# Optimization experiments

Measured on AMD Instinct MI355X. Metric: run time of the kernel, lower is better.

## Reference

```python
import jax, jax.numpy as jnp
import numpy as np

LEAKY_SLOPE = 0.2
MASK_VAL = -9e15


def setup_inputs() -> dict:
    key = jax.random.key(0)
    k1, k2, k3, k4, k5, k6 = jax.random.split(key, 6)
    N_ex, N_kc, F_in, F_out = 20000, 1024, 128, 128
    exercise_h = jax.random.normal(k1, (N_ex, F_in), dtype=jnp.float32)
    kc_h = jax.random.normal(k2, (N_kc, F_in), dtype=jnp.float32)
    adj_exercise_kc = jax.random.randint(k3, (N_ex, N_kc), 0, 2, dtype=jnp.int32)
    # learned params (kaiming-ish scale)
    W1 = jax.random.normal(k4, (F_in, F_out), dtype=jnp.float32) * np.sqrt(2.0 / F_in)
    E = jax.random.normal(k5, (F_in, F_out), dtype=jnp.float32) * np.sqrt(2.0 / F_in)
    a = jax.random.normal(k6, (2 * F_out, 1), dtype=jnp.float32) * np.sqrt(2.0 / (2 * F_out))
    return {"exercise_h": exercise_h, "kc_h": kc_h,
            "adj_exercise_kc": adj_exercise_kc, "W1": W1, "E": E, "a": a}


def reference(exercise_h, kc_h, adj_exercise_kc, W1, E, a):
    F_out = W1.shape[1]
    kc_Wh = kc_h @ W1              # [N_kc, F_out]
    ex_Wh = exercise_h @ W1        # [N_ex, F_out]
    # Decompose a into halves: cat([ex_Wh_i, kc_Wh_j]) @ a == ex_Wh_i@a1 + kc_Wh_j@a2.
    a1, a2 = a[:F_out, 0], a[F_out:, 0]
    e = jax.nn.leaky_relu(ex_Wh @ a1[:, None] + (kc_Wh @ a2)[None, :],
                          negative_slope=LEAKY_SLOPE)   # [N_ex, N_kc]
    e = jnp.where(adj_exercise_kc > 0, e, MASK_VAL)
    attention = jax.nn.softmax(e, axis=1)
    new_kc_embed = attention @ kc_Wh               # [N_ex, F_out]
    exercise_Eh = exercise_h @ E                   # mode == 2
    return jax.nn.elu(new_kc_embed * exercise_Eh)
```

## Files before the change

### kernel.cpp

```cpp
#include <hip/hip_runtime.h>
#include <math.h>

#define N_EXC   20000
#define N_KCC   1024
#define FDIM    128
#define LEAKY_S 0.2f

#define BR  32
#define TJ  64
#define EXS 136
#define WST 72

typedef unsigned short ushort_t;
typedef __attribute__((ext_vector_type(8))) short short8;
typedef __attribute__((ext_vector_type(4))) float floatx4;

__device__ __forceinline__ ushort_t f2bf(float f) {
    unsigned u = __float_as_uint(f);
    u += 0x7FFF + ((u >> 16) & 1);
    return (ushort_t)(u >> 16);
}

__device__ __forceinline__ void async16(const void* g, void* l) {
    __builtin_amdgcn_global_load_lds(
        (const __attribute__((address_space(1))) unsigned int*)g,
        (__attribute__((address_space(3))) unsigned int*)l,
        16, 0, 0);
}


__global__ __launch_bounds__(256) void gat_prep0(const float* __restrict__ W1,
                                                 const float* __restrict__ E,
                                                 const float* __restrict__ a,
                                                 float* __restrict__ ws)
{
    float* w1a1 = ws + N_KCC;
    ushort_t* kc_sw  = (ushort_t*)(ws + N_KCC + FDIM);
    ushort_t* E_sw   = kc_sw + FDIM * N_KCC;
    ushort_t* W1T_sw = E_sw + FDIM * FDIM;
    const int tid = threadIdx.x;

    if (blockIdx.x == 1) {
        #pragma unroll
        for (int u = 0; u < 8; ++u) {
            int ch = u * 256 + tid;
            int half = ch >> 10;
            int rem = ch & 1023;
            int n = rem >> 3, cpp = rem & 7;
            int c = cpp ^ (n & 7);
            int kbase = half * 64 + c * 8;
            unsigned pk[4];
            #pragma unroll
            for (int i = 0; i < 4; ++i) {
                float e0 = E[(kbase + 2 * i + 0) * FDIM + n];
                float e1 = E[(kbase + 2 * i + 1) * FDIM + n];
                pk[i] = (unsigned)f2bf(e0) | ((unsigned)f2bf(e1) << 16);
            }
            *(uint4*)(E_sw + ch * 8) = make_uint4(pk[0], pk[1], pk[2], pk[3]);
        }
        return;
    }

    __shared__ __align__(16) float w1f[128 * 132];
    __shared__ float a_lds[2 * FDIM];
    #pragma unroll
    for (int u = 0; u < 16; ++u) {
        int flat = u * 256 + tid;
        int k = flat >> 5, c4 = (flat & 31) * 4;
        float4 v = *(const float4*)(W1 + k * FDIM + c4);
        w1f[k * 132 + c4 + 0] = v.x; w1f[k * 132 + c4 + 1] = v.y;
        w1f[k * 132 + c4 + 2] = v.z; w1f[k * 132 + c4 + 3] = v.w;
    }
    a_lds[tid] = a[tid];
    __syncthreads();
    #pragma unroll
    for (int u = 0; u < 8; ++u) {
        int ch = u * 256 + tid;
        int f = ch >> 4, c = ch & 15;
        unsigned pk[4];
        #pragma unroll
        for (int i = 0; i < 4; ++i) {
            float v0 = w1f[(c * 8 + 2 * i + 0) * 132 + f];
            float v1 = w1f[(c * 8 + 2 * i + 1) * 132 + f];
            pk[i] = (unsigned)f2bf(v0) | ((unsigned)f2bf(v1) << 16);
        }
        *(uint4*)(W1T_sw + f * 128 + (c ^ (f & 15)) * 8) = make_uint4(pk[0], pk[1], pk[2], pk[3]);
    }
    if (tid < FDIM) {
        float acc = 0.f;
        #pragma unroll 8
        for (int f = 0; f < FDIM; ++f) acc += w1f[tid * 132 + f] * a_lds[f];
        w1a1[tid] = acc;
    }
}

__global__ __launch_bounds__(256) void gat_prep1(const float* __restrict__ kc_h,
                                                 const float* __restrict__ a,
                                                 float* __restrict__ ws)
{
    float* tarr = ws;
    ushort_t* kc_sw  = (ushort_t*)(ws + N_KCC + FDIM);
    ushort_t* E_sw   = kc_sw + FDIM * N_KCC;
    const ushort_t* W1T_sw = E_sw + FDIM * FDIM;

    __shared__ __align__(16) ushort_t w1t[128 * 128];
    __shared__ __align__(16) ushort_t outt[128 * 16];
    __shared__ float a2_lds[FDIM];
    __shared__ float scrT[256];

    const int tid = threadIdx.x;
    const int b = blockIdx.x;
    const int j0 = b * 16;
    const int jt = b >> 2;
    const int c0 = (b & 3) * 2;
    const int lane = tid & 63, w = tid >> 6;
    const int l15 = lane & 15, quad = lane >> 4;

    #pragma unroll
    for (int u = 0; u < 8; ++u) {
        int ci = u * 256 + tid;
        async16(W1T_sw + ci * 8, w1t + ci * 8);
    }
    if (tid < FDIM) a2_lds[tid] = a[FDIM + tid];

    short8 bfrag[4];
    #pragma unroll
    for (int kk = 0; kk < 4; ++kk) {
        const float* p = kc_h + (size_t)(j0 + l15) * FDIM + kk * 32 + quad * 8;
        float4 x = *(const float4*)(p);
        float4 y = *(const float4*)(p + 4);
        float v[8] = {x.x, x.y, x.z, x.w, y.x, y.y, y.z, y.w};
        unsigned pk[4];
        #pragma unroll
        for (int i = 0; i < 4; ++i)
            pk[i] = (unsigned)f2bf(v[2 * i]) | ((unsigned)f2bf(v[2 * i + 1]) << 16);
        uint4 q = make_uint4(pk[0], pk[1], pk[2], pk[3]);
        bfrag[kk] = *(const short8*)&q;
    }
    __syncthreads();

    floatx4 acc[2];
    acc[0] = (floatx4){0.f, 0.f, 0.f, 0.f};
    acc[1] = (floatx4){0.f, 0.f, 0.f, 0.f};
    #pragma unroll
    for (int kk = 0; kk < 4; ++kk) {
        #pragma unroll
        for (int g = 0; g < 2; ++g) {
            int f = w * 32 + g * 16 + l15;
            int cp = (kk * 4 + quad) ^ l15;
            short8 af = *(const short8*)(w1t + f * 128 + cp * 8);
            acc[g] = __builtin_amdgcn_mfma_f32_16x16x32_bf16(af, bfrag[kk], acc[g], 0, 0, 0);
        }
    }

    float tp = 0.f;
    #pragma unroll
    for (int g = 0; g < 2; ++g)
        #pragma unroll
        for (int reg = 0; reg < 4; ++reg) {
            int f = w * 32 + g * 16 + quad * 4 + reg;
            outt[f * 16 + l15] = f2bf(acc[g][reg]);
            tp += acc[g][reg] * a2_lds[f];
        }
    scrT[l15 * 16 + w * 4 + quad] = tp;
    __syncthreads();

    {
        int f = tid >> 1, hf = tid & 1;
        uint4 v = *(const uint4*)(outt + f * 16 + hf * 8);
        int cp = (c0 + hf) ^ (f & 7);
        *(uint4*)(kc_sw + (size_t)jt * 8192 + f * 64 + cp * 8) = v;
    }
    if (tid < 16) {
        float s = 0.f;
        #pragma unroll
        for (int p = 0; p < 16; ++p) s += scrT[tid * 16 + p];
        tarr[j0 + tid] = s;
    }
}

__global__ __launch_bounds__(256, 3) void gat_main(const float* __restrict__ ex_h,
                                                   const int* __restrict__ adj,
                                                   const float* __restrict__ ws,
                                                   float* __restrict__ out)
{
    const float* tarr = ws;
    const float* w1a1 = ws + N_KCC;
    const ushort_t* kc_sw = (const ushort_t*)(ws + N_KCC + FDIM);
    const ushort_t* E_sw  = kc_sw + FDIM * N_KCC;

    __shared__ __align__(16) float t_lds[N_KCC];
    __shared__ __align__(16) ushort_t kc_lds[2 * 8192];
    __shared__ __align__(16) ushort_t ww_lds[4608];
    __shared__ __align__(16) float scrA[256];
    __shared__ __align__(16) float scrB[256];
    __shared__ float w1a1_lds[FDIM];
    __shared__ float s_lds[BR], m_lds[BR], denom_lds[BR];

    const int tid  = threadIdx.x;
    const int R0   = blockIdx.x * BR;
    const int lane = tid & 63, wid = tid >> 6;
    const int l15  = lane & 15, quad = lane >> 4;

    #pragma unroll
    for (int u = 0; u < 8; ++u) {
        int ci = u * 256 + tid;
        async16(E_sw + ci * 8, kc_lds + ci * 8);
    }

    #pragma unroll
    for (int u = 0; u < 4; ++u) t_lds[u * 256 + tid] = tarr[u * 256 + tid];
    if (tid < FDIM) w1a1_lds[tid] = w1a1[tid];
    const int r0 = tid >> 3;
    const int fc = (tid & 7) * 16;
    float exv[16];
    {
        const float* src = ex_h + (size_t)(R0 + r0) * FDIM + fc;
        #pragma unroll
        for (int c = 0; c < 4; ++c) {
            float4 v = *(const float4*)(src + c * 4);
            exv[c * 4 + 0] = v.x; exv[c * 4 + 1] = v.y;
            exv[c * 4 + 2] = v.z; exv[c * 4 + 3] = v.w;
        }
        unsigned pk[8];
        #pragma unroll
        for (int i = 0; i < 8; ++i)
            pk[i] = (unsigned)f2bf(exv[2 * i]) | ((unsigned)f2bf(exv[2 * i + 1]) << 16);
        *(uint4*)(ww_lds + r0 * EXS + fc)     = make_uint4(pk[0], pk[1], pk[2], pk[3]);
        *(uint4*)(ww_lds + r0 * EXS + fc + 8) = make_uint4(pk[4], pk[5], pk[6], pk[7]);
    }

    const int r_w = tid >> 3;
    const int jg  = tid & 7;
    const int* abase = adj + (size_t)(R0 + r_w) * N_KCC + jg * 8;
    unsigned msk[4];
    #pragma unroll
    for (int g = 0; g < 4; ++g) {
        int4 q0 = *(const int4*)(abase + (g * 4 + 0) * 64);
        int4 q1 = *(const int4*)(abase + (g * 4 + 0) * 64 + 4);
        int4 q2 = *(const int4*)(abase + (g * 4 + 1) * 64);
        int4 q3 = *(const int4*)(abase + (g * 4 + 1) * 64 + 4);
        int4 q4 = *(const int4*)(abase + (g * 4 + 2) * 64);
        int4 q5 = *(const int4*)(abase + (g * 4 + 2) * 64 + 4);
        int4 q6 = *(const int4*)(abase + (g * 4 + 3) * 64);
        int4 q7 = *(const int4*)(abase + (g * 4 + 3) * 64 + 4);
        unsigned m = 0;
        m |= (q0.x > 0 ? 1u : 0u) << 0;  m |= (q0.y > 0 ? 1u : 0u) << 1;
        m |= (q0.z > 0 ? 1u : 0u) << 2;  m |= (q0.w > 0 ? 1u : 0u) << 3;
        m |= (q1.x > 0 ? 1u : 0u) << 4;  m |= (q1.y > 0 ? 1u : 0u) << 5;
        m |= (q1.z > 0 ? 1u : 0u) << 6;  m |= (q1.w > 0 ? 1u : 0u) << 7;
        m |= (q2.x > 0 ? 1u : 0u) << 8;  m |= (q2.y > 0 ? 1u : 0u) << 9;
        m |= (q2.z > 0 ? 1u : 0u) << 10; m |= (q2.w > 0 ? 1u : 0u) << 11;
        m |= (q3.x > 0 ? 1u : 0u) << 12; m |= (q3.y > 0 ? 1u : 0u) << 13;
        m |= (q3.z > 0 ? 1u : 0u) << 14; m |= (q3.w > 0 ? 1u : 0u) << 15;
        m |= (q4.x > 0 ? 1u : 0u) << 16; m |= (q4.y > 0 ? 1u : 0u) << 17;
        m |= (q4.z > 0 ? 1u : 0u) << 18; m |= (q4.w > 0 ? 1u : 0u) << 19;
        m |= (q5.x > 0 ? 1u : 0u) << 20; m |= (q5.y > 0 ? 1u : 0u) << 21;
        m |= (q5.z > 0 ? 1u : 0u) << 22; m |= (q5.w > 0 ? 1u : 0u) << 23;
        m |= (q6.x > 0 ? 1u : 0u) << 24; m |= (q6.y > 0 ? 1u : 0u) << 25;
        m |= (q6.z > 0 ? 1u : 0u) << 26; m |= (q6.w > 0 ? 1u : 0u) << 27;
        m |= (q7.x > 0 ? 1u : 0u) << 28; m |= (q7.y > 0 ? 1u : 0u) << 29;
        m |= (q7.z > 0 ? 1u : 0u) << 30; m |= (q7.w > 0 ? 1u : 0u) << 31;
        msk[g] = m;
    }
    __syncthreads();

    {
        float mx = fmaxf(fmaxf(t_lds[tid], t_lds[256 + tid]),
                         fmaxf(t_lds[512 + tid], t_lds[768 + tid]));
        scrB[tid] = mx;
        float p = 0.f;
        #pragma unroll
        for (int i = 0; i < 16; ++i) p += exv[i] * w1a1_lds[fc + i];
        scrA[tid] = p;
    }
    __syncthreads();
    if (tid < 64)
        scrB[tid] = fmaxf(fmaxf(scrB[tid], scrB[tid + 64]),
                          fmaxf(scrB[tid + 128], scrB[tid + 192]));
    __syncthreads();
    if (tid < BR) {
        float Tm = scrB[0];
        #pragma unroll 8
        for (int i = 1; i < 64; ++i) Tm = fmaxf(Tm, scrB[i]);
        float s = 0.f;
        #pragma unroll
        for (int g = 0; g < 8; ++g) s += scrA[tid * 8 + g];
        s_lds[tid] = s;
        float x = s + Tm;
        m_lds[tid] = (x >= 0.f) ? x : LEAKY_S * x;
    }
    __syncthreads();

    floatx4 eh_acc[2][2], att_acc[2][2];
    #pragma unroll
    for (int mg = 0; mg < 2; ++mg)
        #pragma unroll
        for (int h = 0; h < 2; ++h) {
            eh_acc[mg][h]  = (floatx4){0.f, 0.f, 0.f, 0.f};
            att_acc[mg][h] = (floatx4){0.f, 0.f, 0.f, 0.f};
        }
    #pragma unroll
    for (int kk = 0; kk < 4; ++kk) {
        short8 a0 = *(const short8*)(ww_lds + l15 * EXS + kk * 32 + quad * 8);
        short8 a1 = *(const short8*)(ww_lds + (16 + l15) * EXS + kk * 32 + quad * 8);
        #pragma unroll
        for (int h = 0; h < 2; ++h) {
            const int n = (h * 4 + wid) * 16 + l15;
            const int cpp = ((kk & 1) * 4 + quad) ^ (n & 7);
            short8 bf = *(const short8*)(kc_lds + (kk >> 1) * 8192 + n * 64 + cpp * 8);
            eh_acc[0][h] = __builtin_amdgcn_mfma_f32_16x16x32_bf16(a0, bf, eh_acc[0][h], 0, 0, 0);
            eh_acc[1][h] = __builtin_amdgcn_mfma_f32_16x16x32_bf16(a1, bf, eh_acc[1][h], 0, 0, 0);
        }
    }
    __syncthreads();

    const float sr = s_lds[r_w];
    const float mr = m_lds[r_w];
    float denom_part = 0.f;

    auto genw = [&](int jt, ushort_t* wb) {
        const int jb = jt * TJ + jg * 8;
        float4 ta = *(const float4*)(t_lds + jb);
        float4 tb = *(const float4*)(t_lds + jb + 4);
        float tv[8] = {ta.x, ta.y, ta.z, ta.w, tb.x, tb.y, tb.z, tb.w};
        unsigned mb = msk[jt >> 2] >> ((jt & 3) * 8);
        float wv[8];
        #pragma unroll
        for (int e = 0; e < 8; ++e) {
            float x = sr + tv[e];
            x = fmaxf(x, LEAKY_S * x);
            float w = __expf(x - mr);
            w = ((mb >> e) & 1u) ? w : 0.f;
            denom_part += w;
            wv[e] = w;
        }
        unsigned pk[4];
        #pragma unroll
        for (int i = 0; i < 4; ++i) {
            unsigned ua = __float_as_uint(wv[2 * i + 0]) + 0x8000u;
            unsigned ub = __float_as_uint(wv[2 * i + 1]) + 0x8000u;
            pk[i] = __builtin_amdgcn_perm(ub, ua, 0x07060302);
        }
        *(uint4*)(wb + r_w * WST + jg * 8) = make_uint4(pk[0], pk[1], pk[2], pk[3]);
    };

    #pragma unroll
    for (int u = 0; u < 4; ++u) {
        int ci = u * 256 + tid;
        async16(kc_sw + ci * 8, kc_lds + ci * 8);
    }
    genw(0, ww_lds);
    __syncthreads();

    for (int jt = 0; jt < N_KCC / TJ; ++jt) {
        if (jt < 15) {
            const ushort_t* gsrc = kc_sw + (size_t)(jt + 1) * 8192;
            ushort_t* kdst = kc_lds + ((jt + 1) & 1) * 8192;
            #pragma unroll
            for (int u = 0; u < 4; ++u) {
                int ci = u * 256 + tid;
                async16(gsrc + ci * 8, kdst + ci * 8);
            }
            genw(jt + 1, ww_lds + ((jt + 1) & 1) * 2304);
        }
        const ushort_t* kcb = kc_lds + (jt & 1) * 8192;
        const ushort_t* wb  = ww_lds + (jt & 1) * 2304;
        #pragma unroll
        for (int kk = 0; kk < 2; ++kk) {
            short8 a0 = *(const short8*)(wb + l15 * WST + kk * 32 + quad * 8);
            short8 a1 = *(const short8*)(wb + (16 + l15) * WST + kk * 32 + quad * 8);
            #pragma unroll
            for (int h = 0; h < 2; ++h) {
                const int f = (h * 4 + wid) * 16 + l15;
                const int cpp = (kk * 4 + quad) ^ (f & 7);
                short8 bf = *(const short8*)(kcb + f * 64 + cpp * 8);
                att_acc[0][h] = __builtin_amdgcn_mfma_f32_16x16x32_bf16(a0, bf, att_acc[0][h], 0, 0, 0);
                att_acc[1][h] = __builtin_amdgcn_mfma_f32_16x16x32_bf16(a1, bf, att_acc[1][h], 0, 0, 0);
            }
        }
        __syncthreads();
    }

    scrA[tid] = denom_part;
    __syncthreads();
    if (tid < BR) {
        float d = 0.f;
        #pragma unroll
        for (int g = 0; g < 8; ++g) d += scrA[tid * 8 + g];
        denom_lds[tid] = (d > 0.f) ? d : 1.f;
    }
    __syncthreads();

    #pragma unroll
    for (int mg = 0; mg < 2; ++mg) {
        float rd[4];
        #pragma unroll
        for (int reg = 0; reg < 4; ++reg)
            rd[reg] = 1.f / denom_lds[mg * 16 + quad * 4 + reg];
        #pragma unroll
        for (int h = 0; h < 2; ++h) {
            const int col = (h * 4 + wid) * 16 + l15;
            #pragma unroll
            for (int reg = 0; reg < 4; ++reg) {
                const int rl = mg * 16 + quad * 4 + reg;
                float v = att_acc[mg][h][reg] * rd[reg] * eh_acc[mg][h][reg];
                out[(size_t)(R0 + rl) * FDIM + col] = (v > 0.f) ? v : expm1f(v);
            }
        }
    }
}

extern "C" void kernel_launch(void* const* d_in, const int* in_sizes, int n_in,
                              void* d_out, int out_size, void* d_ws, size_t ws_size,
                              hipStream_t stream)
{
    const float* ex_h = (const float*)d_in[0];
    const float* kc_h = (const float*)d_in[1];
    const int*   adj  = (const int*)d_in[2];
    const float* W1   = (const float*)d_in[3];
    const float* E    = (const float*)d_in[4];
    const float* a    = (const float*)d_in[5];
    float* outp = (float*)d_out;
    float* ws   = (float*)d_ws;

    gat_prep0<<<2, 256, 0, stream>>>(W1, E, a, ws);
    gat_prep1<<<64, 256, 0, stream>>>(kc_h, a, ws);
    gat_main<<<N_EXC / BR, 256, 0, stream>>>(ex_h, adj, ws, outp);
}
```

Before: 168.4 us.

## Pre-pack adjacency into bitmasks in a separate kernel before main attention

```diff
diff --git a/kernel.cpp b/kernel.cpp
--- a/kernel.cpp
+++ b/kernel.cpp
@@ -28,6 +28,43 @@
         16, 0, 0);
 }
 
+
+__global__ __launch_bounds__(256) void gat_adj(const int* __restrict__ adj,
+                                               float* __restrict__ ws)
+{
+    ushort_t* kc_sw  = (ushort_t*)(ws + N_KCC + FDIM);
+    ushort_t* E_sw   = kc_sw + FDIM * N_KCC;
+    ushort_t* W1T_sw = E_sw + FDIM * FDIM;
+    unsigned* msk_sw = (unsigned*)(W1T_sw + FDIM * FDIM);
+
+    __shared__ unsigned char ml[8 * 8 * 16];
+
+    const int tid = threadIdx.x;
+    const int r_loc = tid >> 5, seg = tid & 31;
+    const size_t r = (size_t)blockIdx.x * 8 + r_loc;
+    const int4* p = (const int4*)(adj + r * N_KCC + seg * 32);
+    const int jt = seg >> 1;
+    #pragma unroll
+    for (int q = 0; q < 4; ++q) {
+        int4 a0 = p[q * 2 + 0];
+        int4 a1 = p[q * 2 + 1];
+        unsigned m = (a0.x > 0 ? 1u : 0u)
+                   | (a0.y > 0 ? 2u : 0u)
+                   | (a0.z > 0 ? 4u : 0u)
+                   | (a0.w > 0 ? 8u : 0u)
+                   | (a1.x > 0 ? 16u : 0u)
+                   | (a1.y > 0 ? 32u : 0u)
+                   | (a1.z > 0 ? 64u : 0u)
+                   | (a1.w > 0 ? 128u : 0u);
+        int jg = (seg & 1) * 4 + q;
+        ml[(r_loc * 8 + jg) * 16 + jt] = (unsigned char)m;
+    }
+    __syncthreads();
+    if (tid < 64) {
+        uint4 v = *(const uint4*)(ml + tid * 16);
+        *(uint4*)(msk_sw + (size_t)blockIdx.x * 256 + tid * 4) = v;
+    }
+}
 
 __global__ __launch_bounds__(256) void gat_prep0(const float* __restrict__ W1,
                                                  const float* __restrict__ E,
@@ -180,7 +217,6 @@
 }
 
 __global__ __launch_bounds__(256, 3) void gat_main(const float* __restrict__ ex_h,
-                                                   const int* __restrict__ adj,
                                                    const float* __restrict__ ws,
                                                    float* __restrict__ out)
 {
@@ -188,6 +224,8 @@
     const float* w1a1 = ws + N_KCC;
     const ushort_t* kc_sw = (const ushort_t*)(ws + N_KCC + FDIM);
     const ushort_t* E_sw  = kc_sw + FDIM * N_KCC;
+    const ushort_t* W1T_sw = E_sw + FDIM * FDIM;
+    const unsigned* msk_sw = (const unsigned*)(W1T_sw + FDIM * FDIM);
 
     __shared__ __align__(16) float t_lds[N_KCC];
     __shared__ __align__(16) ushort_t kc_lds[2 * 8192];
@@ -232,36 +270,10 @@
 
     const int r_w = tid >> 3;
     const int jg  = tid & 7;
-    const int* abase = adj + (size_t)(R0 + r_w) * N_KCC + jg * 8;
     unsigned msk[4];
-    #pragma unroll
-    for (int g = 0; g < 4; ++g) {
-        int4 q0 = *(const int4*)(abase + (g * 4 + 0) * 64);
-        int4 q1 = *(const int4*)(abase + (g * 4 + 0) * 64 + 4);
-        int4 q2 = *(const int4*)(abase + (g * 4 + 1) * 64);
-        int4 q3 = *(const int4*)(abase + (g * 4 + 1) * 64 + 4);
-        int4 q4 = *(const int4*)(abase + (g * 4 + 2) * 64);
-        int4 q5 = *(const int4*)(abase + (g * 4 + 2) * 64 + 4);
-        int4 q6 = *(const int4*)(abase + (g * 4 + 3) * 64);
-        int4 q7 = *(const int4*)(abase + (g * 4 + 3) * 64 + 4);
-        unsigned m = 0;
-        m |= (q0.x > 0 ? 1u : 0u) << 0;  m |= (q0.y > 0 ? 1u : 0u) << 1;
-        m |= (q0.z > 0 ? 1u : 0u) << 2;  m |= (q0.w > 0 ? 1u : 0u) << 3;
-        m |= (q1.x > 0 ? 1u : 0u) << 4;  m |= (q1.y > 0 ? 1u : 0u) << 5;
-        m |= (q1.z > 0 ? 1u : 0u) << 6;  m |= (q1.w > 0 ? 1u : 0u) << 7;
-        m |= (q2.x > 0 ? 1u : 0u) << 8;  m |= (q2.y > 0 ? 1u : 0u) << 9;
-        m |= (q2.z > 0 ? 1u : 0u) << 10; m |= (q2.w > 0 ? 1u : 0u) << 11;
-        m |= (q3.x > 0 ? 1u : 0u) << 12; m |= (q3.y > 0 ? 1u : 0u) << 13;
-        m |= (q3.z > 0 ? 1u : 0u) << 14; m |= (q3.w > 0 ? 1u : 0u) << 15;
-        m |= (q4.x > 0 ? 1u : 0u) << 16; m |= (q4.y > 0 ? 1u : 0u) << 17;
-        m |= (q4.z > 0 ? 1u : 0u) << 18; m |= (q4.w > 0 ? 1u : 0u) << 19;
-        m |= (q5.x > 0 ? 1u : 0u) << 20; m |= (q5.y > 0 ? 1u : 0u) << 21;
-        m |= (q5.z > 0 ? 1u : 0u) << 22; m |= (q5.w > 0 ? 1u : 0u) << 23;
-        m |= (q6.x > 0 ? 1u : 0u) << 24; m |= (q6.y > 0 ? 1u : 0u) << 25;
-        m |= (q6.z > 0 ? 1u : 0u) << 26; m |= (q6.w > 0 ? 1u : 0u) << 27;
-        m |= (q7.x > 0 ? 1u : 0u) << 28; m |= (q7.y > 0 ? 1u : 0u) << 29;
-        m |= (q7.z > 0 ? 1u : 0u) << 30; m |= (q7.w > 0 ? 1u : 0u) << 31;
-        msk[g] = m;
+    {
+        uint4 mv = *(const uint4*)(msk_sw + ((size_t)(R0 + r_w) * 8 + jg) * 4);
+        msk[0] = mv.x; msk[1] = mv.y; msk[2] = mv.z; msk[3] = mv.w;
     }
     __syncthreads();
 
@@ -424,7 +436,8 @@
     float* outp = (float*)d_out;
     float* ws   = (float*)d_ws;
 
+    gat_adj<<<N_EXC / 8, 256, 0, stream>>>(adj, ws);
     gat_prep0<<<2, 256, 0, stream>>>(W1, E, a, ws);
     gat_prep1<<<64, 256, 0, stream>>>(kc_h, a, ws);
-    gat_main<<<N_EXC / BR, 256, 0, stream>>>(ex_h, adj, ws, outp);
-}
+    gat_main<<<N_EXC / BR, 256, 0, stream>>>(ex_h, ws, outp);
+}
```

Measured after the change: 173.5 us. +3.1%, slower.
